# Kernel tuning notes

Hardware: AMD Instinct MI355X
Metric: run time of the kernel (lower is better)

## Reference

```python
import jax, jax.numpy as jnp
import numpy as np

E = 512        # embedding_dim
HEADS = 8
PD = 32        # patch_dim
STRIDE = 16    # unfold stride (hard-coded in source)
P = 16         # max regions per image (padded)
NCLS = 3       # num_classes
LN_EPS = 1e-5


def layer_norm(x, g, b):
    mu = x.mean(-1, keepdims=True)
    v = ((x - mu) ** 2).mean(-1, keepdims=True)
    return (x - mu) / jnp.sqrt(v + LN_EPS) * g + b


def patch2vec(x, Wr, br):
    # x: [N, C, PD, PD]; AdaptiveAvgPool3d to (C//4, PD//2, PD//2) with exact
    # integer ratios == block-mean pooling, then Linear(fvector, E).
    N, C, H, W = x.shape
    y = x.reshape(N, C // 4, 4, H // 2, 2, W // 2, 2).mean(axis=(2, 4, 6))
    return y.reshape(N, -1) @ Wr.T + br


def mha(q_in, kv_in, Wqkv, bqkv, Wo, bo):
    # torch nn.MultiheadAttention, batch_first=True
    B, Pq, _ = q_in.shape
    L = kv_in.shape[1]
    hd = E // HEADS
    Wq, Wk, Wv = Wqkv[:E], Wqkv[E:2 * E], Wqkv[2 * E:]
    bq, bk, bv = bqkv[:E], bqkv[E:2 * E], bqkv[2 * E:]
    q = (q_in @ Wq.T + bq).reshape(B, Pq, HEADS, hd)
    k = (kv_in @ Wk.T + bk).reshape(B, L, HEADS, hd)
    v = (kv_in @ Wv.T + bv).reshape(B, L, HEADS, hd)
    scores = jnp.einsum('bphd,blhd->bhpl', q, k) / jnp.sqrt(jnp.asarray(hd, q.dtype))
    attn = jax.nn.softmax(scores, axis=-1)
    out = jnp.einsum('bhpl,blhd->bphd', attn, v).reshape(B, Pq, E)
    return out @ Wo.T + bo


def setup_inputs() -> dict:
    key = jax.random.key(0)
    ks = jax.random.split(key, 12)
    B, C, H, W = 8, 64, 256, 256
    fv = (C // 4) * (PD // 2) * (PD // 2)  # 4096
    s = lambda n: 1.0 / np.sqrt(n)
    return {
        'features': jax.random.normal(ks[0], (B, C, H, W), jnp.float32),
        'probs': jax.random.uniform(ks[1], (B, NCLS, H, W), jnp.float32),
        'patches': jax.random.normal(ks[2], (B, P, C, PD, PD), jnp.float32),
        'masks': jax.random.randint(ks[3], (B, H, W), 0, P + 1, jnp.int32),
        'ln_g': jnp.ones((E,), jnp.float32),
        'ln_b': jnp.zeros((E,), jnp.float32),
        'Wr': jax.random.normal(ks[4], (E, fv), jnp.float32) * s(fv),
        'br': jnp.zeros((E,), jnp.float32),
        'Wqkv': jax.random.normal(ks[5], (3 * E, E), jnp.float32) * s(E),
        'bqkv': jnp.zeros((3 * E,), jnp.float32),
        'Wo': jax.random.normal(ks[6], (E, E), jnp.float32) * s(E),
        'bo': jnp.zeros((E,), jnp.float32),
        'Wm': jax.random.normal(ks[7], (E, E), jnp.float32) * s(E),
        'bm': jnp.zeros((E,), jnp.float32),
        'Wc': jax.random.normal(ks[8], (NCLS - 1, E), jnp.float32) * s(E),
        'bc': jnp.zeros((NCLS - 1,), jnp.float32),
    }


def reference(features, probs, patches, masks, ln_g, ln_b, Wr, br,
              Wqkv, bqkv, Wo, bo, Wm, bm, Wc, bc):
    B, C, H, W = features.shape
    # ---- unfold features into overlapping PDxPD blocks, stride 16 ----
    n = (H - PD) // STRIDE + 1  # 15
    rows = (jnp.arange(n) * STRIDE)[:, None] + jnp.arange(PD)[None, :]  # [n, PD]
    xb = features[:, :, rows, :]          # [B, C, n, PD, W]
    blocks = xb[:, :, :, :, rows]         # [B, C, n, PD, n, PD]
    blocks = blocks.transpose(0, 2, 4, 1, 3, 5).reshape(B, n * n, C, PD, PD)
    L = n * n

    # ---- shared Patch2vec embedding + shared LayerNorm ----
    pe = layer_norm(patch2vec(patches.reshape(B * P, C, PD, PD), Wr, br).reshape(B, P, E), ln_g, ln_b)
    be = layer_norm(patch2vec(blocks.reshape(B * L, C, PD, PD), Wr, br).reshape(B, L, E), ln_g, ln_b)

    # ---- attention + residual MLP ----
    attn = mha(pe, be, Wqkv, bqkv, Wo, bo)
    res = layer_norm(attn + pe, ln_g, ln_b)
    x = jax.nn.gelu(res @ Wm.T + bm, approximate=False) + res
    outs = x @ Wc.T + bc  # [B, P, 2]

    # ---- vectorized masked reclassify (regions are disjoint) ----
    labels = masks  # [B, H, W], 0 = background, 1..P = regions
    seg = (labels.astype(jnp.int32) + jnp.arange(B, dtype=jnp.int32)[:, None, None] * (P + 1)).reshape(-1)
    pr = probs.transpose(0, 2, 3, 1).reshape(-1, NCLS)
    sums = jax.ops.segment_sum(pr, seg, num_segments=B * (P + 1)).reshape(B, P + 1, NCLS)
    cnt = jax.ops.segment_sum(jnp.ones((pr.shape[0],), pr.dtype), seg, num_segments=B * (P + 1)).reshape(B, P + 1)
    mean = sums / jnp.maximum(cnt, 1.0)[..., None] + 1e-6  # orig_mean_logits per region
    ml = mean[:, 1:, :]  # [B, P, NCLS], region labels 1..P <-> logits 0..P-1
    new0 = ml[..., 0] / (0.5 * (ml[..., 1] + ml[..., 2])) * outs.mean(-1)
    newv = jnp.stack([new0, outs[..., 0], outs[..., 1]], axis=-1)  # [B, P, 3]
    newv_full = jnp.concatenate([jnp.zeros((B, 1, NCLS), newv.dtype), newv], axis=1)
    vals = newv_full[jnp.arange(B)[:, None], labels.reshape(B, -1)]  # [B, H*W, 3]
    vals = vals.reshape(B, H, W, NCLS).transpose(0, 3, 1, 2)
    return jnp.where((labels > 0)[:, None, :, :], vals, probs)
```

## Files before the change

kernel.cpp:

```cpp
#include <hip/hip_runtime.h>
#include <stdint.h>


typedef __attribute__((ext_vector_type(8))) short bf16x8;
typedef __attribute__((ext_vector_type(4))) float f32x4;

__device__ __forceinline__ unsigned short f2bf(float x) {
    union { float f; unsigned u; } v; v.f = x;
    unsigned r = v.u + 0x7FFFu + ((v.u >> 16) & 1u);
    return (unsigned short)(r >> 16);
}
__device__ __forceinline__ float bf2f(unsigned short x) {
    union { unsigned u; float f; } v; v.u = ((unsigned)x) << 16; return v.f;
}

__device__ __forceinline__ void g2l16(const unsigned short* g, unsigned short* l) {
    __builtin_amdgcn_global_load_lds(
        (const __attribute__((address_space(1))) unsigned int*)g,
        (__attribute__((address_space(3))) unsigned int*)l, 16, 0, 0);
}

__global__ __launch_bounds__(256) void k_prep(
    const float* __restrict__ f, const float* __restrict__ p,
    const float* __restrict__ Wr, const float* __restrict__ Wqkv,
    const float* __restrict__ Wo, const float* __restrict__ Wm,
    unsigned short* __restrict__ gp, unsigned short* __restrict__ Xb,
    unsigned short* __restrict__ oWr, unsigned short* __restrict__ oWqkv,
    unsigned short* __restrict__ oWo, unsigned short* __restrict__ oWm,
    float* __restrict__ seg)
{
    int blk = blockIdx.x, tid = threadIdx.x;
    if (blk < 4096) {
        if (blk == 0) for (int i = tid; i < 544; i += 256) seg[i] = 0.f;
        unsigned t = blk * 256u + tid;
        unsigned q2 = t & 63u, r = (t >> 6) & 127u, g = (t >> 13) & 15u, b = t >> 17;
        const float4* f4 = (const float4*)f;
        float s0 = 0.f, s1 = 0.f;
        unsigned cb = b * 64u + g * 4u;
#pragma unroll
        for (int j = 0; j < 4; ++j)
#pragma unroll
            for (int a = 0; a < 2; ++a) {
                float4 v = f4[((cb + j) * 256u + 2u * r + a) * 64u + q2];
                s0 += v.x + v.y; s1 += v.z + v.w;
            }
        ushort2 o; o.x = f2bf(s0 * 0.0625f); o.y = f2bf(s1 * 0.0625f);
        ((ushort2*)gp)[((b * 16u + g) * 128u + r) * 64u + q2] = o;
    } else if (blk < 6144) {
        unsigned t = (blk - 4096) * 256u + tid;
        unsigned i = t & 4095u, row = t >> 12;
        unsigned q = i & 15u, r = (i >> 4) & 15u, g = i >> 8;
        const float2* p2 = (const float2*)p;
        float s = 0.f;
        unsigned cb = row * 64u + g * 4u;
#pragma unroll
        for (int j = 0; j < 4; ++j)
#pragma unroll
            for (int a = 0; a < 2; ++a) {
                unsigned idx = ((cb + j) * 32u + 2u * r + a) * 32u + 2u * q;
                float2 v = p2[idx >> 1];
                s += v.x + v.y;
            }
        Xb[(size_t)row * 4096 + i] = f2bf(s * 0.0625f);
    } else {
        int t = (blk - 6144) * 256 + tid;
        const float* src; unsigned short* dst; int i;
        if (t < 524288)      { src = Wr;   dst = oWr;   i = t; }
        else if (t < 720896) { src = Wqkv; dst = oWqkv; i = t - 524288; }
        else if (t < 786432) { src = Wo;   dst = oWo;   i = t - 720896; }
        else                 { src = Wm;   dst = oWm;   i = t - 786432; }
        float4 v = ((const float4*)src)[i];
        ushort4 o;
        o.x = f2bf(v.x); o.y = f2bf(v.y); o.z = f2bf(v.z); o.w = f2bf(v.w);
        ((ushort4*)dst)[i] = o;
    }
}

template<bool GATHER, bool BF16OUT>
__global__ __launch_bounds__(256) void k_gemm128(
    const unsigned short* __restrict__ A, const unsigned short* __restrict__ Gp,
    const unsigned short* __restrict__ Bw,
    const float* __restrict__ bias, float* __restrict__ C,
    unsigned short* __restrict__ Cb,
    int M, int N, int K, int klen)
{
    __shared__ __align__(16) unsigned short As[128 * 32];
    __shared__ __align__(16) unsigned short Bs[128 * 32];
    const int tid = threadIdx.x, w = tid >> 6, lane = tid & 63;
    const int nt = blockIdx.x, mt = blockIdx.y, ks = blockIdx.z;
    const int kbase = ks * klen;
    const int l15 = lane & 15, kq = (lane >> 4) * 8;
    const int wm = (w >> 1) * 64, wn = (w & 1) * 64;
    const int srow0 = w * 32, lrow = lane >> 2, lcol = (lane & 3) * 8;

    size_t arowbase[2]; bool apatch[2];
#pragma unroll
    for (int c = 0; c < 2; ++c) {
        int r = srow0 + c * 16 + lrow;
        int ga = mt * 128 + r; if (ga > M - 1) ga = M - 1;
        if (GATHER && ga >= 128) {
            int rr = ga - 128;
            int bb = rr / 225, ij = rr - bb * 225;
            int ii = ij / 15, jj = ij - ii * 15;
            arowbase[c] = (size_t)bb * 262144 + ii * 1024 + jj * 8;
            apatch[c] = false;
        } else {
            arowbase[c] = (size_t)ga * K;
            apatch[c] = true;
        }
    }
    const int brow0 = nt * 128;

    f32x4 acc[4][4];
#pragma unroll
    for (int i = 0; i < 4; ++i)
#pragma unroll
        for (int j = 0; j < 4; ++j) acc[i][j] = (f32x4){0.f, 0.f, 0.f, 0.f};

    for (int k0 = 0; k0 < klen; k0 += 32) {
        int kcol = kbase + k0 + lcol;
#pragma unroll
        for (int c = 0; c < 2; ++c) {
            const unsigned short* gp_a;
            if (!GATHER || apatch[c]) {
                gp_a = A + arowbase[c] + kcol;
            } else {
                gp_a = Gp + arowbase[c] + ((size_t)(kcol >> 8) << 14)
                     + (((kcol >> 4) & 15) << 7) + (kcol & 15);
            }
            g2l16(gp_a, &As[(srow0 + c * 16) * 32]);
            g2l16(Bw + (size_t)(brow0 + srow0 + c * 16 + lrow) * K + kcol,
                  &Bs[(srow0 + c * 16) * 32]);
        }
        __syncthreads();
        bf16x8 af[4], bf[4];
#pragma unroll
        for (int i = 0; i < 4; ++i) {
            af[i] = *(const bf16x8*)&As[(wm + 16 * i + l15) * 32 + kq];
            bf[i] = *(const bf16x8*)&Bs[(wn + 16 * i + l15) * 32 + kq];
        }
#pragma unroll
        for (int i = 0; i < 4; ++i)
#pragma unroll
            for (int j = 0; j < 4; ++j)
                acc[i][j] = __builtin_amdgcn_mfma_f32_16x16x32_bf16(af[i], bf[j], acc[i][j], 0, 0, 0);
        __syncthreads();
    }
    float* Cp = C + (size_t)ks * M * N;
#pragma unroll
    for (int i = 0; i < 4; ++i) {
        int rowb = mt * 128 + wm + i * 16 + (lane >> 4) * 4;
#pragma unroll
        for (int j = 0; j < 4; ++j) {
            int col = nt * 128 + wn + j * 16 + l15;
            float bv = bias ? bias[col] : 0.f;
#pragma unroll
            for (int r = 0; r < 4; ++r) {
                int row = rowb + r;
                if (row < M) {
                    if (BF16OUT) Cb[(size_t)row * N + col] = f2bf(acc[i][j][r] + bv);
                    else         Cp[(size_t)row * N + col] = acc[i][j][r] + bv;
                }
            }
        }
    }
}

__global__ __launch_bounds__(256) void k_lnred(
    const float* __restrict__ Yp, const float* __restrict__ br,
    const float* __restrict__ gg, const float* __restrict__ bb,
    float* __restrict__ outF, unsigned short* __restrict__ outB,
    int rows, int nsplit)
{
    int wave = threadIdx.x >> 6, lane = threadIdx.x & 63;
    int row = blockIdx.x * 4 + wave;
    if (row >= rows) return;
    size_t base = (size_t)row * 512 + lane * 8;
    float v[8];
    { const float* bp = br + lane * 8;
      float4 a = *(const float4*)bp, b = *(const float4*)(bp + 4);
      v[0]=a.x; v[1]=a.y; v[2]=a.z; v[3]=a.w; v[4]=b.x; v[5]=b.y; v[6]=b.z; v[7]=b.w; }
    for (int s = 0; s < nsplit; ++s) {
        const float* xp = Yp + (size_t)s * rows * 512 + base;
        float4 a = *(const float4*)xp, b = *(const float4*)(xp + 4);
        v[0]+=a.x; v[1]+=a.y; v[2]+=a.z; v[3]+=a.w; v[4]+=b.x; v[5]+=b.y; v[6]+=b.z; v[7]+=b.w;
    }
    float s = 0.f;
#pragma unroll
    for (int i = 0; i < 8; ++i) s += v[i];
#pragma unroll
    for (int m = 32; m; m >>= 1) s += __shfl_xor(s, m, 64);
    float mu = s * (1.f / 512.f);
    float sq = 0.f;
#pragma unroll
    for (int i = 0; i < 8; ++i) { float d = v[i] - mu; sq += d * d; }
#pragma unroll
    for (int m = 32; m; m >>= 1) sq += __shfl_xor(sq, m, 64);
    float rstd = rsqrtf(sq * (1.f / 512.f) + 1e-5f);
    const float* gp = gg + lane * 8;
    const float* bp2 = bb + lane * 8;
    float4 g0 = *(const float4*)gp, g1 = *(const float4*)(gp + 4);
    float4 b0 = *(const float4*)bp2, b1 = *(const float4*)(bp2 + 4);
    float ga[8] = {g0.x,g0.y,g0.z,g0.w,g1.x,g1.y,g1.z,g1.w};
    float ba[8] = {b0.x,b0.y,b0.z,b0.w,b1.x,b1.y,b1.z,b1.w};
    float o[8];
#pragma unroll
    for (int i = 0; i < 8; ++i) o[i] = (v[i] - mu) * rstd * ga[i] + ba[i];
    if (row < 128) {
        float* ofp = outF + base;
        float4 w0; w0.x=o[0]; w0.y=o[1]; w0.z=o[2]; w0.w=o[3];
        float4 w1; w1.x=o[4]; w1.y=o[5]; w1.z=o[6]; w1.w=o[7];
        *(float4*)ofp = w0; *(float4*)(ofp + 4) = w1;
    }
    unsigned short* obp = outB + base;
    ushort4 u0, u1;
    u0.x=f2bf(o[0]); u0.y=f2bf(o[1]); u0.z=f2bf(o[2]); u0.w=f2bf(o[3]);
    u1.x=f2bf(o[4]); u1.y=f2bf(o[5]); u1.z=f2bf(o[6]); u1.w=f2bf(o[7]);
    ((ushort4*)obp)[0] = u0; ((ushort4*)obp)[1] = u1;
}

__global__ __launch_bounds__(256) void k_attn(
    const unsigned short* __restrict__ QKVb, unsigned short* __restrict__ attn_bf)
{
    const int b = blockIdx.x, h = blockIdx.y, pz = blockIdx.z;
    __shared__ __align__(16) float qs[4 * 64];
    __shared__ __align__(16) unsigned short Ks[225 * 68];
    __shared__ __align__(16) unsigned short Vs[225 * 64];
    __shared__ float sc[4 * 225];
    const int t = threadIdx.x;

    {
        int p = t >> 6, d = t & 63;
        qs[t] = bf2f(QKVb[(size_t)(b * 16 + pz * 4 + p) * 1536 + h * 64 + d]);
    }
    for (int i = t; i < 1800; i += 256) {
        int l = i >> 3, d8 = (i & 7) * 8;
        size_t base = (size_t)(128 + b * 225 + l) * 1536 + h * 64 + d8;
        uint4 kk4 = *(const uint4*)(QKVb + base + 512);
        *(uint2*)&Ks[l * 68 + d8]     = make_uint2(kk4.x, kk4.y);
        *(uint2*)&Ks[l * 68 + d8 + 4] = make_uint2(kk4.z, kk4.w);
        *(uint4*)&Vs[l * 64 + d8] = *(const uint4*)(QKVb + base + 1024);
    }
    __syncthreads();
    for (int i = t; i < 900; i += 256) {
        int p = i / 225, l = i - p * 225;
        const ushort4* k4 = (const ushort4*)&Ks[l * 68];
        const float4* q4 = (const float4*)&qs[p * 64];
        float s = 0.f;
#pragma unroll
        for (int d = 0; d < 16; ++d) {
            ushort4 kk = k4[d]; float4 qq = q4[d];
            s += bf2f(kk.x) * qq.x + bf2f(kk.y) * qq.y
               + bf2f(kk.z) * qq.z + bf2f(kk.w) * qq.w;
        }
        sc[p * 225 + l] = s * 0.125f;
    }
    __syncthreads();
    const int lane = t & 63, wave = t >> 6;
    {
        float* row = &sc[wave * 225];
        float m = -1e30f;
        for (int l = lane; l < 225; l += 64) m = fmaxf(m, row[l]);
#pragma unroll
        for (int off = 32; off; off >>= 1) m = fmaxf(m, __shfl_xor(m, off, 64));
        float s = 0.f;
        for (int l = lane; l < 225; l += 64) { float e = __expf(row[l] - m); row[l] = e; s += e; }
#pragma unroll
        for (int off = 32; off; off >>= 1) s += __shfl_xor(s, off, 64);
        float inv = 1.f / s;
        for (int l = lane; l < 225; l += 64) row[l] *= inv;
    }
    __syncthreads();
    {
        float o = 0.f;
        const float* scp = &sc[wave * 225];
        for (int l = 0; l < 225; ++l) o += scp[l] * bf2f(Vs[l * 64 + lane]);
        attn_bf[(size_t)(b * 16 + pz * 4 + wave) * 512 + h * 64 + lane] = f2bf(o);
    }
}

__global__ __launch_bounds__(256) void k_tail(
    const unsigned short* __restrict__ attnb, const unsigned short* __restrict__ Wo_b,
    const float* __restrict__ bo, const float* __restrict__ LNf,
    const float* __restrict__ gg, const float* __restrict__ bb,
    const unsigned short* __restrict__ Wm_b, const float* __restrict__ bm,
    const float* __restrict__ Wc, const float* __restrict__ bc,
    float* __restrict__ outs)
{
    __shared__ __align__(16) unsigned short Abuf[16 * 520];
    __shared__ __align__(16) unsigned short Bs[4][128 * 64];
    __shared__ float Zf[16 * 512];
    __shared__ float part[16][4][2];
    const int tid = threadIdx.x, w = tid >> 6, lane = tid & 63;
    const int l15 = lane & 15, quad = lane >> 4, kq = quad * 8;
    const int r0 = blockIdx.x * 16;

#pragma unroll
    for (int c = 0; c < 4; ++c) {
        int row = c * 4 + w;
        g2l16(attnb + (size_t)(r0 + row) * 512 + lane * 8, &Abuf[row * 520]);
    }

    f32x4 acc[8];
#pragma unroll
    for (int i = 0; i < 8; ++i) acc[i] = (f32x4){0.f, 0.f, 0.f, 0.f};

    for (int k0 = 0; k0 < 512; k0 += 64) {
#pragma unroll
        for (int c = 0; c < 16; ++c) {
            int n = w * 128 + c * 8 + (lane >> 3);
            g2l16(Wo_b + (size_t)n * 512 + k0 + (lane & 7) * 8, &Bs[w][c * 512]);
        }
        __syncthreads();
        bf16x8 af0 = *(const bf16x8*)&Abuf[l15 * 520 + k0 + kq];
        bf16x8 af1 = *(const bf16x8*)&Abuf[l15 * 520 + k0 + 32 + kq];
#pragma unroll
        for (int i = 0; i < 8; ++i) {
            bf16x8 b0 = *(const bf16x8*)&Bs[w][(i * 16 + l15) * 64 + kq];
            bf16x8 b1 = *(const bf16x8*)&Bs[w][(i * 16 + l15) * 64 + 32 + kq];
            acc[i] = __builtin_amdgcn_mfma_f32_16x16x32_bf16(af0, b0, acc[i], 0, 0, 0);
            acc[i] = __builtin_amdgcn_mfma_f32_16x16x32_bf16(af1, b1, acc[i], 0, 0, 0);
        }
        __syncthreads();
    }
#pragma unroll
    for (int i = 0; i < 8; ++i) {
        int col = w * 128 + i * 16 + l15;
        float bv = bo[col];
#pragma unroll
        for (int r = 0; r < 4; ++r)
            Zf[(quad * 4 + r) * 512 + col] = acc[i][r] + bv;
    }
    __syncthreads();

    for (int pass = 0; pass < 4; ++pass) {
        int row = pass * 4 + w;
        float v[8];
#pragma unroll
        for (int i = 0; i < 8; ++i)
            v[i] = Zf[row * 512 + lane * 8 + i] + LNf[(size_t)(r0 + row) * 512 + lane * 8 + i];
        float s = 0.f;
#pragma unroll
        for (int i = 0; i < 8; ++i) s += v[i];
#pragma unroll
        for (int m = 32; m; m >>= 1) s += __shfl_xor(s, m, 64);
        float mu = s * (1.f / 512.f);
        float sq = 0.f;
#pragma unroll
        for (int i = 0; i < 8; ++i) { float d = v[i] - mu; sq += d * d; }
#pragma unroll
        for (int m = 32; m; m >>= 1) sq += __shfl_xor(sq, m, 64);
        float rstd = rsqrtf(sq * (1.f / 512.f) + 1e-5f);
#pragma unroll
        for (int i = 0; i < 8; ++i) {
            int col = lane * 8 + i;
            float o = (v[i] - mu) * rstd * gg[col] + bb[col];
            Zf[row * 512 + col] = o;
            Abuf[row * 520 + col] = f2bf(o);
        }
    }
    __syncthreads();

#pragma unroll
    for (int i = 0; i < 8; ++i) acc[i] = (f32x4){0.f, 0.f, 0.f, 0.f};
    for (int k0 = 0; k0 < 512; k0 += 64) {
#pragma unroll
        for (int c = 0; c < 16; ++c) {
            int n = w * 128 + c * 8 + (lane >> 3);
            g2l16(Wm_b + (size_t)n * 512 + k0 + (lane & 7) * 8, &Bs[w][c * 512]);
        }
        __syncthreads();
        bf16x8 af0 = *(const bf16x8*)&Abuf[l15 * 520 + k0 + kq];
        bf16x8 af1 = *(const bf16x8*)&Abuf[l15 * 520 + k0 + 32 + kq];
#pragma unroll
        for (int i = 0; i < 8; ++i) {
            bf16x8 b0 = *(const bf16x8*)&Bs[w][(i * 16 + l15) * 64 + kq];
            bf16x8 b1 = *(const bf16x8*)&Bs[w][(i * 16 + l15) * 64 + 32 + kq];
            acc[i] = __builtin_amdgcn_mfma_f32_16x16x32_bf16(af0, b0, acc[i], 0, 0, 0);
            acc[i] = __builtin_amdgcn_mfma_f32_16x16x32_bf16(af1, b1, acc[i], 0, 0, 0);
        }
        __syncthreads();
    }
    float s0[4] = {0,0,0,0}, s1[4] = {0,0,0,0};
#pragma unroll
    for (int i = 0; i < 8; ++i) {
        int col = w * 128 + i * 16 + l15;
        float wc0 = Wc[col], wc1 = Wc[512 + col], bmv = bm[col];
#pragma unroll
        for (int r = 0; r < 4; ++r) {
            float v = acc[i][r] + bmv;
            float x = 0.5f * v * (1.f + erff(v * 0.70710678118654752f))
                    + Zf[(quad * 4 + r) * 512 + col];
            s0[r] += x * wc0; s1[r] += x * wc1;
        }
    }
#pragma unroll
    for (int off = 8; off; off >>= 1)
#pragma unroll
        for (int r = 0; r < 4; ++r) {
            s0[r] += __shfl_xor(s0[r], off, 16);
            s1[r] += __shfl_xor(s1[r], off, 16);
        }
    if (l15 == 0)
#pragma unroll
        for (int r = 0; r < 4; ++r) {
            part[quad * 4 + r][w][0] = s0[r];
            part[quad * 4 + r][w][1] = s1[r];
        }
    __syncthreads();
    if (tid < 32) {
        int row = tid >> 1, c = tid & 1;
        float s = part[row][0][c] + part[row][1][c] + part[row][2][c] + part[row][3][c];
        outs[(r0 + row) * 2 + c] = s + bc[c];
    }
}

__global__ __launch_bounds__(256) void k_hist(
    const int* __restrict__ masks, const float* __restrict__ probs,
    float* __restrict__ sums, float* __restrict__ cnt)
{
    __shared__ float ls[4][68];
    int t = threadIdx.x, wave = t >> 6;
    for (int i = t; i < 272; i += 256) ((float*)ls)[i] = 0.f;
    __syncthreads();
    int b = blockIdx.x >> 6, chunk = blockIdx.x & 63;
    int base = chunk * 1024;
    for (int it = 0; it < 4; ++it) {
        int px = base + it * 256 + t;
        int lab = masks[b * 65536 + px];
        atomicAdd(&ls[wave][lab * 3 + 0], probs[(size_t)(b * 3 + 0) * 65536 + px]);
        atomicAdd(&ls[wave][lab * 3 + 1], probs[(size_t)(b * 3 + 1) * 65536 + px]);
        atomicAdd(&ls[wave][lab * 3 + 2], probs[(size_t)(b * 3 + 2) * 65536 + px]);
        atomicAdd(&ls[wave][51 + lab], 1.f);
    }
    __syncthreads();
    if (t < 68) {
        float v = ls[0][t] + ls[1][t] + ls[2][t] + ls[3][t];
        if (t < 51) atomicAdd(&sums[b * 51 + t], v);
        else        atomicAdd(&cnt[b * 17 + t - 51], v);
    }
}

__global__ __launch_bounds__(256) void k_out(
    const int* __restrict__ masks, const float* __restrict__ probs,
    const float* __restrict__ seg, const float* __restrict__ outs,
    float* __restrict__ out)
{
    __shared__ float nv[17 * 3];
    int tid = threadIdx.x;
    int b = blockIdx.x >> 8;
    if (tid < 17) {
        int lab = tid;
        if (lab == 0) { nv[0] = 0.f; nv[1] = 0.f; nv[2] = 0.f; }
        else {
            float c  = fmaxf(seg[408 + b * 17 + lab], 1.f);
            float m0 = seg[(b * 17 + lab) * 3 + 0] / c + 1e-6f;
            float m1 = seg[(b * 17 + lab) * 3 + 1] / c + 1e-6f;
            float m2 = seg[(b * 17 + lab) * 3 + 2] / c + 1e-6f;
            int p = lab - 1;
            float o0 = outs[(b * 16 + p) * 2 + 0], o1 = outs[(b * 16 + p) * 2 + 1];
            nv[lab * 3 + 0] = m0 / (0.5f * (m1 + m2)) * (0.5f * (o0 + o1));
            nv[lab * 3 + 1] = o0;
            nv[lab * 3 + 2] = o1;
        }
    }
    __syncthreads();
    int px = (blockIdx.x & 255) * 256 + tid;
    int gl = b * 65536 + px;
    int lab = masks[gl];
    if (lab > 0) {
        out[(size_t)(b*3+0)*65536 + px] = nv[lab*3+0];
        out[(size_t)(b*3+1)*65536 + px] = nv[lab*3+1];
        out[(size_t)(b*3+2)*65536 + px] = nv[lab*3+2];
    } else {
        out[(size_t)(b*3+0)*65536 + px] = probs[(size_t)(b*3+0)*65536 + px];
        out[(size_t)(b*3+1)*65536 + px] = probs[(size_t)(b*3+1)*65536 + px];
        out[(size_t)(b*3+2)*65536 + px] = probs[(size_t)(b*3+2)*65536 + px];
    }
}

extern "C" void kernel_launch(void* const* d_in, const int* in_sizes, int n_in,
                              void* d_out, int out_size, void* d_ws, size_t ws_size,
                              hipStream_t stream)
{
    const float* features = (const float*)d_in[0];
    const float* probs    = (const float*)d_in[1];
    const float* patches  = (const float*)d_in[2];
    const int*   masks    = (const int*)d_in[3];
    const float* ln_g     = (const float*)d_in[4];
    const float* ln_b     = (const float*)d_in[5];
    const float* Wr       = (const float*)d_in[6];
    const float* br       = (const float*)d_in[7];
    const float* Wqkv     = (const float*)d_in[8];
    const float* bqkv     = (const float*)d_in[9];
    const float* Wo       = (const float*)d_in[10];
    const float* bo       = (const float*)d_in[11];
    const float* Wm       = (const float*)d_in[12];
    const float* bm       = (const float*)d_in[13];
    const float* Wc       = (const float*)d_in[14];
    const float* bc       = (const float*)d_in[15];
    float* out = (float*)d_out;

    char* w = (char*)d_ws;
    size_t off = 0;
    auto alloc = [&](size_t bytes) -> char* {
        char* p = w + off;
        off += (bytes + 255) & ~(size_t)255;
        return p;
    };
    unsigned short* Gp     = (unsigned short*)alloc((size_t)2097152 * 2);
    unsigned short* Xb     = (unsigned short*)alloc((size_t)128 * 4096 * 2);
    unsigned short* Wr_b   = (unsigned short*)alloc((size_t)2097152 * 2);
    unsigned short* Wqkv_b = (unsigned short*)alloc((size_t)786432 * 2);
    unsigned short* Wo_b   = (unsigned short*)alloc((size_t)262144 * 2);
    unsigned short* Wm_b   = (unsigned short*)alloc((size_t)262144 * 2);
    float* Yp   = (float*)alloc((size_t)8 * 1928 * 512 * 4);
    float* LNf  = (float*)alloc((size_t)128 * 512 * 4);
    unsigned short* LNb  = (unsigned short*)alloc((size_t)1928 * 512 * 2);
    unsigned short* QKVb = (unsigned short*)alloc((size_t)1928 * 1536 * 2);
    unsigned short* attnb = (unsigned short*)alloc((size_t)65536 * 2);
    float* outsB = (float*)alloc((size_t)256 * 4);
    float* seg   = (float*)alloc((size_t)544 * 4);

    k_prep<<<9472, 256, 0, stream>>>(features, patches, Wr, Wqkv, Wo, Wm,
                                     Gp, Xb, Wr_b, Wqkv_b, Wo_b, Wm_b, seg);
    k_hist<<<512, 256, 0, stream>>>(masks, probs, seg, seg + 408);
    k_gemm128<true, false><<<dim3(4, 16, 8), 256, 0, stream>>>(
        Xb, Gp, Wr_b, nullptr, Yp, nullptr, 1928, 512, 4096, 512);
    k_lnred<<<482, 256, 0, stream>>>(Yp, br, ln_g, ln_b, LNf, LNb, 1928, 8);
    k_gemm128<false, true><<<dim3(12, 16, 1), 256, 0, stream>>>(
        LNb, nullptr, Wqkv_b, bqkv, nullptr, QKVb, 1928, 1536, 512, 512);
    k_attn<<<dim3(8, 8, 4), 256, 0, stream>>>(QKVb, attnb);
    k_tail<<<8, 256, 0, stream>>>(attnb, Wo_b, bo, LNf, ln_g, ln_b,
                                  Wm_b, bm, Wc, bc, outsB);
    k_out<<<2048, 256, 0, stream>>>(masks, probs, seg, outsB, out);
}
```

Measured before the change: 363.0 us.

## Fuse histogram into prep kernel and use 64x64 tiles for QKV GEMM

The per-region histogram becomes extra blocks of the prep kernel. Those blocks write per-chunk partials instead of global atomics, and the output kernel reduces the partials itself, which removes one launch, the seg zeroing and the global atomics. The QKV projection moves from a 128x128-tile GEMM with 192 blocks to a dedicated 64x64-tile kernel with 744 blocks, aiming for better CU occupancy on the small problem. The cost is that every k_out block re-reduces 64 partials, and the smaller tiles reuse data less.

```diff
diff --git a/kernel.cpp b/kernel.cpp
--- a/kernel.cpp
+++ b/kernel.cpp
@@ -24,14 +24,14 @@
     const float* __restrict__ f, const float* __restrict__ p,
     const float* __restrict__ Wr, const float* __restrict__ Wqkv,
     const float* __restrict__ Wo, const float* __restrict__ Wm,
+    const int* __restrict__ masks, const float* __restrict__ probs,
     unsigned short* __restrict__ gp, unsigned short* __restrict__ Xb,
     unsigned short* __restrict__ oWr, unsigned short* __restrict__ oWqkv,
     unsigned short* __restrict__ oWo, unsigned short* __restrict__ oWm,
-    float* __restrict__ seg)
+    float* __restrict__ hpart)
 {
     int blk = blockIdx.x, tid = threadIdx.x;
     if (blk < 4096) {
-        if (blk == 0) for (int i = tid; i < 544; i += 256) seg[i] = 0.f;
         unsigned t = blk * 256u + tid;
         unsigned q2 = t & 63u, r = (t >> 6) & 127u, g = (t >> 13) & 15u, b = t >> 17;
         const float4* f4 = (const float4*)f;
@@ -62,7 +62,7 @@
                 s += v.x + v.y;
             }
         Xb[(size_t)row * 4096 + i] = f2bf(s * 0.0625f);
-    } else {
+    } else if (blk < 9472) {
         int t = (blk - 6144) * 256 + tid;
         const float* src; unsigned short* dst; int i;
         if (t < 524288)      { src = Wr;   dst = oWr;   i = t; }
@@ -73,16 +73,33 @@
         ushort4 o;
         o.x = f2bf(v.x); o.y = f2bf(v.y); o.z = f2bf(v.z); o.w = f2bf(v.w);
         ((ushort4*)dst)[i] = o;
-    }
-}
-
-template<bool GATHER, bool BF16OUT>
+    } else {
+        __shared__ float ls[4][68];
+        int hb = blk - 9472;
+        int b = hb >> 6, chunk = hb & 63;
+        int wave = tid >> 6;
+        for (int i = tid; i < 272; i += 256) ((float*)ls)[i] = 0.f;
+        __syncthreads();
+        int base = chunk * 1024;
+        for (int it = 0; it < 4; ++it) {
+            int px = base + it * 256 + tid;
+            int lab = masks[b * 65536 + px];
+            atomicAdd(&ls[wave][lab * 3 + 0], probs[(size_t)(b * 3 + 0) * 65536 + px]);
+            atomicAdd(&ls[wave][lab * 3 + 1], probs[(size_t)(b * 3 + 1) * 65536 + px]);
+            atomicAdd(&ls[wave][lab * 3 + 2], probs[(size_t)(b * 3 + 2) * 65536 + px]);
+            atomicAdd(&ls[wave][51 + lab], 1.f);
+        }
+        __syncthreads();
+        if (tid < 68)
+            hpart[(size_t)hb * 68 + tid] = ls[0][tid] + ls[1][tid] + ls[2][tid] + ls[3][tid];
+    }
+}
+
+template<bool GATHER>
 __global__ __launch_bounds__(256) void k_gemm128(
     const unsigned short* __restrict__ A, const unsigned short* __restrict__ Gp,
     const unsigned short* __restrict__ Bw,
-    const float* __restrict__ bias, float* __restrict__ C,
-    unsigned short* __restrict__ Cb,
-    int M, int N, int K, int klen)
+    float* __restrict__ C, int M, int N, int K, int klen)
 {
     __shared__ __align__(16) unsigned short As[128 * 32];
     __shared__ __align__(16) unsigned short Bs[128 * 32];
@@ -153,14 +170,62 @@
 #pragma unroll
         for (int j = 0; j < 4; ++j) {
             int col = nt * 128 + wn + j * 16 + l15;
-            float bv = bias ? bias[col] : 0.f;
 #pragma unroll
             for (int r = 0; r < 4; ++r) {
                 int row = rowb + r;
-                if (row < M) {
-                    if (BF16OUT) Cb[(size_t)row * N + col] = f2bf(acc[i][j][r] + bv);
-                    else         Cp[(size_t)row * N + col] = acc[i][j][r] + bv;
-                }
+                if (row < M) Cp[(size_t)row * N + col] = acc[i][j][r];
+            }
+        }
+    }
+}
+
+__global__ __launch_bounds__(256) void k_gemm64(
+    const unsigned short* __restrict__ A, const unsigned short* __restrict__ Bw,
+    const float* __restrict__ bias, unsigned short* __restrict__ Cb,
+    int M, int N, int K)
+{
+    __shared__ __align__(16) unsigned short As[64 * 32];
+    __shared__ __align__(16) unsigned short Bs[64 * 32];
+    const int tid = threadIdx.x, w = tid >> 6, lane = tid & 63;
+    const int bm = blockIdx.y, bn = blockIdx.x;
+    const int wm = (w >> 1) * 32, wn = (w & 1) * 32;
+    const int l15 = lane & 15, kq = (lane >> 4) * 8;
+    const int lrow = lane >> 2, lcol = (lane & 3) * 8;
+    int ga = bm * 64 + w * 16 + lrow; if (ga > M - 1) ga = M - 1;
+    const unsigned short* Ap = A + (size_t)ga * K;
+    const unsigned short* Bp = Bw + (size_t)(bn * 64 + w * 16 + lrow) * K;
+
+    f32x4 acc[2][2];
+#pragma unroll
+    for (int i = 0; i < 2; ++i)
+#pragma unroll
+        for (int j = 0; j < 2; ++j) acc[i][j] = (f32x4){0.f, 0.f, 0.f, 0.f};
+
+    for (int k0 = 0; k0 < K; k0 += 32) {
+        g2l16(Ap + k0 + lcol, &As[(w * 16) * 32]);
+        g2l16(Bp + k0 + lcol, &Bs[(w * 16) * 32]);
+        __syncthreads();
+        bf16x8 a0 = *(const bf16x8*)&As[(wm + l15) * 32 + kq];
+        bf16x8 a1 = *(const bf16x8*)&As[(wm + 16 + l15) * 32 + kq];
+        bf16x8 b0 = *(const bf16x8*)&Bs[(wn + l15) * 32 + kq];
+        bf16x8 b1 = *(const bf16x8*)&Bs[(wn + 16 + l15) * 32 + kq];
+        acc[0][0] = __builtin_amdgcn_mfma_f32_16x16x32_bf16(a0, b0, acc[0][0], 0, 0, 0);
+        acc[0][1] = __builtin_amdgcn_mfma_f32_16x16x32_bf16(a0, b1, acc[0][1], 0, 0, 0);
+        acc[1][0] = __builtin_amdgcn_mfma_f32_16x16x32_bf16(a1, b0, acc[1][0], 0, 0, 0);
+        acc[1][1] = __builtin_amdgcn_mfma_f32_16x16x32_bf16(a1, b1, acc[1][1], 0, 0, 0);
+        __syncthreads();
+    }
+#pragma unroll
+    for (int it = 0; it < 2; ++it) {
+        int rowb = bm * 64 + wm + it * 16 + (lane >> 4) * 4;
+#pragma unroll
+        for (int iu = 0; iu < 2; ++iu) {
+            int col = bn * 64 + wn + iu * 16 + l15;
+            float bv = bias[col];
+#pragma unroll
+            for (int r = 0; r < 4; ++r) {
+                int row = rowb + r;
+                if (row < M) Cb[(size_t)row * N + col] = f2bf(acc[it][iu][r] + bv);
             }
         }
     }
@@ -415,48 +480,30 @@
     }
 }
 
-__global__ __launch_bounds__(256) void k_hist(
-    const int* __restrict__ masks, const float* __restrict__ probs,
-    float* __restrict__ sums, float* __restrict__ cnt)
-{
-    __shared__ float ls[4][68];
-    int t = threadIdx.x, wave = t >> 6;
-    for (int i = t; i < 272; i += 256) ((float*)ls)[i] = 0.f;
-    __syncthreads();
-    int b = blockIdx.x >> 6, chunk = blockIdx.x & 63;
-    int base = chunk * 1024;
-    for (int it = 0; it < 4; ++it) {
-        int px = base + it * 256 + t;
-        int lab = masks[b * 65536 + px];
-        atomicAdd(&ls[wave][lab * 3 + 0], probs[(size_t)(b * 3 + 0) * 65536 + px]);
-        atomicAdd(&ls[wave][lab * 3 + 1], probs[(size_t)(b * 3 + 1) * 65536 + px]);
-        atomicAdd(&ls[wave][lab * 3 + 2], probs[(size_t)(b * 3 + 2) * 65536 + px]);
-        atomicAdd(&ls[wave][51 + lab], 1.f);
-    }
-    __syncthreads();
-    if (t < 68) {
-        float v = ls[0][t] + ls[1][t] + ls[2][t] + ls[3][t];
-        if (t < 51) atomicAdd(&sums[b * 51 + t], v);
-        else        atomicAdd(&cnt[b * 17 + t - 51], v);
-    }
-}
-
 __global__ __launch_bounds__(256) void k_out(
     const int* __restrict__ masks, const float* __restrict__ probs,
-    const float* __restrict__ seg, const float* __restrict__ outs,
+    const float* __restrict__ hpart, const float* __restrict__ outs,
     float* __restrict__ out)
 {
+    __shared__ float ps[68];
     __shared__ float nv[17 * 3];
     int tid = threadIdx.x;
     int b = blockIdx.x >> 8;
+    if (tid < 68) {
+        float s = 0.f;
+        const float* pp = hpart + (size_t)b * 64 * 68 + tid;
+        for (int c = 0; c < 64; ++c) s += pp[c * 68];
+        ps[tid] = s;
+    }
+    __syncthreads();
     if (tid < 17) {
         int lab = tid;
         if (lab == 0) { nv[0] = 0.f; nv[1] = 0.f; nv[2] = 0.f; }
         else {
-            float c  = fmaxf(seg[408 + b * 17 + lab], 1.f);
-            float m0 = seg[(b * 17 + lab) * 3 + 0] / c + 1e-6f;
-            float m1 = seg[(b * 17 + lab) * 3 + 1] / c + 1e-6f;
-            float m2 = seg[(b * 17 + lab) * 3 + 2] / c + 1e-6f;
+            float c  = fmaxf(ps[51 + lab], 1.f);
+            float m0 = ps[lab * 3 + 0] / c + 1e-6f;
+            float m1 = ps[lab * 3 + 1] / c + 1e-6f;
+            float m2 = ps[lab * 3 + 2] / c + 1e-6f;
             int p = lab - 1;
             float o0 = outs[(b * 16 + p) * 2 + 0], o1 = outs[(b * 16 + p) * 2 + 1];
             nv[lab * 3 + 0] = m0 / (0.5f * (m1 + m2)) * (0.5f * (o0 + o1));
@@ -520,18 +567,17 @@
     unsigned short* QKVb = (unsigned short*)alloc((size_t)1928 * 1536 * 2);
     unsigned short* attnb = (unsigned short*)alloc((size_t)65536 * 2);
     float* outsB = (float*)alloc((size_t)256 * 4);
-    float* seg   = (float*)alloc((size_t)544 * 4);
-
-    k_prep<<<9472, 256, 0, stream>>>(features, patches, Wr, Wqkv, Wo, Wm,
-                                     Gp, Xb, Wr_b, Wqkv_b, Wo_b, Wm_b, seg);
-    k_hist<<<512, 256, 0, stream>>>(masks, probs, seg, seg + 408);
-    k_gemm128<true, false><<<dim3(4, 16, 8), 256, 0, stream>>>(
-        Xb, Gp, Wr_b, nullptr, Yp, nullptr, 1928, 512, 4096, 512);
+    float* hpart = (float*)alloc((size_t)512 * 68 * 4);
+
+    k_prep<<<9984, 256, 0, stream>>>(features, patches, Wr, Wqkv, Wo, Wm,
+                                     masks, probs,
+                                     Gp, Xb, Wr_b, Wqkv_b, Wo_b, Wm_b, hpart);
+    k_gemm128<true><<<dim3(4, 16, 8), 256, 0, stream>>>(
+        Xb, Gp, Wr_b, Yp, 1928, 512, 4096, 512);
     k_lnred<<<482, 256, 0, stream>>>(Yp, br, ln_g, ln_b, LNf, LNb, 1928, 8);
-    k_gemm128<false, true><<<dim3(12, 16, 1), 256, 0, stream>>>(
-        LNb, nullptr, Wqkv_b, bqkv, nullptr, QKVb, 1928, 1536, 512, 512);
+    k_gemm64<<<dim3(24, 31), 256, 0, stream>>>(LNb, Wqkv_b, bqkv, QKVb, 1928, 1536, 512);
     k_attn<<<dim3(8, 8, 4), 256, 0, stream>>>(QKVb, attnb);
     k_tail<<<8, 256, 0, stream>>>(attnb, Wo_b, bo, LNf, ln_g, ln_b,
                                   Wm_b, bm, Wc, bc, outsB);
-    k_out<<<2048, 256, 0, stream>>>(masks, probs, seg, outsB, out);
-}
+    k_out<<<2048, 256, 0, stream>>>(masks, probs, hpart, outsB, out);
+}
```

Result: slower. 370.7 us (+2.1%).
